# Performance work log

Measured on AMD Instinct MI355X. Metric: run time of the kernel, lower is better.

The kernel has to match this reference:

```python
import jax, jax.numpy as jnp
import numpy as np

N_NODES = 100000
N_EDGES = 1600000
IN_FEATS = 128
H_FEATS = 64
PROP_STEP = 2


def _gcn_propagate(x, src, dst, num_nodes, add_self_loops):
    """PyG gcn_norm + scatter-add propagation. edge_weight=None -> all ones.
    GCNConv uses add_self_loops=True; LGConv uses add_self_loops=False."""
    if add_self_loops:
        loop = jnp.arange(num_nodes, dtype=src.dtype)
        src = jnp.concatenate([src, loop])
        dst = jnp.concatenate([dst, loop])
    # degree over destination nodes (flow source_to_target)
    deg = jax.ops.segment_sum(jnp.ones(src.shape, dtype=x.dtype), dst,
                              num_segments=num_nodes)
    dinv = jnp.where(deg > 0, jax.lax.rsqrt(deg), jnp.zeros_like(deg))
    norm = dinv[src] * dinv[dst]                      # [E]
    msg = x[src] * norm[:, None]                      # [E, F] gather + scale
    return jax.ops.segment_sum(msg, dst, num_segments=num_nodes)  # [N, F]


def setup_inputs() -> dict:
    key = jax.random.key(0)
    k1, k2, k3 = jax.random.split(key, 3)
    edge_index = jax.random.randint(k1, (2, N_EDGES), 0, N_NODES, dtype=jnp.int32)
    in_feat = jax.random.normal(k2, (N_NODES, IN_FEATS), dtype=jnp.float32)
    # GCNConv linear weight (bias=False), stored as [in, out]
    W1 = jax.random.normal(k3, (IN_FEATS, H_FEATS), dtype=jnp.float32) * (1.0 / np.sqrt(IN_FEATS))
    alphas = jnp.ones((PROP_STEP,), dtype=jnp.float32)  # nn.Parameter(ones(prop_step))
    return {"edge_index": edge_index, "in_feat": in_feat, "W1": W1, "alphas": alphas}


def reference(edge_index, in_feat, W1, alphas):
    src, dst = edge_index[0], edge_index[1]
    num_nodes = in_feat.shape[0]
    alpha = jax.nn.softmax(alphas)
    # conv1 = GCNConv(bias=False): linear transform then normalized propagation with self loops
    h = _gcn_propagate(in_feat @ W1, src, dst, num_nodes, add_self_loops=True)
    res = h * alpha[0]
    # remaining steps: LGConv (no self loops), norm/relu disabled by default
    for i in range(1, PROP_STEP):
        h = _gcn_propagate(h, src, dst, num_nodes, add_self_loops=False)
        res = res + h * alpha[i]
    return res
```

## Files before the change

kernel.cpp:

```cpp
#include <hip/hip_runtime.h>

#define N_NODES 100000
#define N_EDGES 1600000
#define IN_F 128
#define H_F 64
#define ZROW N_NODES

#define BSH 10
#define BNODES 1024
#define NBKT 98
#define EPB 4096
#define BCAP 20000
#define SCAP 28192

typedef short short8 __attribute__((ext_vector_type(8)));
typedef float floatx4 __attribute__((ext_vector_type(4)));

union U16x8 { short8 v; unsigned short us[8]; unsigned int u[4]; };

static __device__ __forceinline__ unsigned short f2bf(float f) {
    unsigned int u = __float_as_uint(f);
    unsigned int r = (u + 0x7FFFu + ((u >> 16) & 1u)) >> 16;
    return (unsigned short)r;
}
static __device__ __forceinline__ float bflo(unsigned int u) {
    return __uint_as_float(u << 16);
}
static __device__ __forceinline__ float bfhi(unsigned int u) {
    return __uint_as_float(u & 0xFFFF0000u);
}
static __device__ __forceinline__ unsigned int pk2(float a, float b) {
    return (unsigned int)f2bf(a) | ((unsigned int)f2bf(b) << 16);
}

__global__ __launch_bounds__(256) void initwpack_kernel(const float* __restrict__ W,
                                                        unsigned int* __restrict__ wfrag,
                                                        int* __restrict__ ccur,
                                                        unsigned int* __restrict__ XsZ,
                                                        unsigned int* __restrict__ h1sZ) {
    int i = blockIdx.x * 256 + threadIdx.x;
    int reg = i & 3, lane = (i >> 2) & 63, fkc = i >> 8;
    int ct = fkc >> 2, kc = fkc & 3;
    int fcol = ct * 16 + (lane & 15);
    int k = kc * 32 + (lane >> 4) * 8 + reg * 2;
    wfrag[i] = pk2(W[k * 64 + fcol], W[(k + 1) * 64 + fcol]);

    if (blockIdx.x == 0) {
        int t = threadIdx.x;
        if (t < NBKT) ccur[t] = t * BCAP;
        if (t < 32) XsZ[t] = 0;
        else if (t < 64) h1sZ[t - 32] = 0;
    }
}

__global__ __launch_bounds__(256) void coarse_scatter_kernel(const int* __restrict__ src,
                                                             const int* __restrict__ dst,
                                                             int* __restrict__ ccur,
                                                             unsigned int* __restrict__ tmp, int E) {
    __shared__ unsigned int buf[EPB];
    __shared__ unsigned char bktA[EPB];
    __shared__ int cnt[NBKT], lofs[NBKT], gofs[NBKT];
    int base = blockIdx.x * EPB;
    int n = E - base; if (n > EPB) n = EPB;

    for (int i = threadIdx.x; i < NBKT; i += 256) cnt[i] = 0;
    __syncthreads();

    unsigned int v[16]; int bk[16], loc[16];
    #pragma unroll
    for (int j = 0; j < 16; ++j) {
        int o = threadIdx.x + j * 256;
        bk[j] = -1;
        if (o < n) {
            int s = src[base + o];
            int d = dst[base + o];
            bk[j]  = d >> BSH;
            v[j]   = ((unsigned int)(d & (BNODES - 1)) << 17) | (unsigned int)s;
            loc[j] = atomicAdd(&cnt[bk[j]], 1);
        }
    }
    __syncthreads();
    if (threadIdx.x == 0) {
        int run = 0;
        for (int b = 0; b < NBKT; ++b) { lofs[b] = run; run += cnt[b]; }
    }
    __syncthreads();
    if (threadIdx.x < NBKT && cnt[threadIdx.x] > 0)
        gofs[threadIdx.x] = atomicAdd(&ccur[threadIdx.x], cnt[threadIdx.x]);
    __syncthreads();
    #pragma unroll
    for (int j = 0; j < 16; ++j)
        if (bk[j] >= 0) {
            int p = lofs[bk[j]] + loc[j];
            buf[p]  = v[j];
            bktA[p] = (unsigned char)bk[j];
        }
    __syncthreads();
    for (int i = threadIdx.x; i < n; i += 256) {
        int b = bktA[i];
        tmp[gofs[b] + (i - lofs[b])] = buf[i];
    }
}

__global__ __launch_bounds__(512) void bucket_kernel(const unsigned int* __restrict__ tmp,
                                                     const int* __restrict__ ccur,
                                                     int* __restrict__ offsets,
                                                     unsigned char* __restrict__ npad8,
                                                     int* __restrict__ sorted_src,
                                                     float* __restrict__ dinv1,
                                                     float* __restrict__ dinv2, int N) {
    __shared__ int cnt[BNODES];
    __shared__ int sd[512];
    int b   = blockIdx.x;
    int tid = threadIdx.x;
    int tbeg = b * BCAP, tend = ccur[b];
    int sbase = b * SCAP;

    for (int i = tid; i < BNODES; i += 512) cnt[i] = 0;
    __syncthreads();
    for (int i = tbeg + tid; i < tend; i += 512)
        atomicAdd(&cnt[tmp[i] >> 17], 1);
    __syncthreads();

    int c0 = cnt[2 * tid], c1 = cnt[2 * tid + 1];
    int p0 = (c0 + 7) & ~7, p1 = (c1 + 7) & ~7;
    int s  = p0 + p1;
    sd[tid] = s;
    __syncthreads();
    for (int off = 1; off < 512; off <<= 1) {
        int t = (tid >= off) ? sd[tid - off] : 0;
        __syncthreads();
        sd[tid] += t;
        __syncthreads();
    }
    int ex = sd[tid] - s;
    int g0 = sbase + ex, g1 = sbase + ex + p0;

    int node0 = b * BNODES + 2 * tid;
    if (node0 < N) {
        offsets[node0] = g0;
        npad8[node0] = (unsigned char)(p0 >> 3);
        dinv1[node0] = rsqrtf((float)(c0 + 1));
        dinv2[node0] = c0 ? rsqrtf((float)c0) : 0.0f;
        for (int k = c0; k < p0; ++k) sorted_src[g0 + k] = ZROW;
    }
    if (node0 + 1 < N) {
        offsets[node0 + 1] = g1;
        npad8[node0 + 1] = (unsigned char)(p1 >> 3);
        dinv1[node0 + 1] = rsqrtf((float)(c1 + 1));
        dinv2[node0 + 1] = c1 ? rsqrtf((float)c1) : 0.0f;
        for (int k = c1; k < p1; ++k) sorted_src[g1 + k] = ZROW;
    }
    __syncthreads();
    cnt[2 * tid] = g0;
    cnt[2 * tid + 1] = g1;
    __syncthreads();

    for (int i = tbeg + tid; i < tend; i += 512) {
        unsigned int v = tmp[i];
        int p = atomicAdd(&cnt[v >> 17], 1);
        sorted_src[p] = (int)(v & 0x1FFFFu);
    }
}

__global__ __launch_bounds__(256) void gemm_kernel(const float* __restrict__ A,
                                                   const uint4* __restrict__ wfrag,
                                                   const float* __restrict__ dinv1,
                                                   unsigned short* __restrict__ Xs, int nTiles) {
    int wid = blockIdx.x * 4 + (threadIdx.x >> 6);
    int lane = threadIdx.x & 63;
    int lrow = lane & 15, lk = lane >> 4;

    short8 wf[16];
    #pragma unroll
    for (int i = 0; i < 16; ++i)
        wf[i] = *reinterpret_cast<const short8*>(&wfrag[i * 64 + lane]);

    #pragma unroll
    for (int tt = 0; tt < 4; ++tt) {
        int t = wid * 4 + tt;
        if (t >= nTiles) break;
        int node = t * 16 + lrow;
        const float4* ap = reinterpret_cast<const float4*>(A + (size_t)node * IN_F);

        short8 af[4];
        #pragma unroll
        for (int kc = 0; kc < 4; ++kc) {
            float4 x = ap[kc * 8 + lk * 2];
            float4 y = ap[kc * 8 + lk * 2 + 1];
            U16x8 u;
            u.us[0] = f2bf(x.x); u.us[1] = f2bf(x.y); u.us[2] = f2bf(x.z); u.us[3] = f2bf(x.w);
            u.us[4] = f2bf(y.x); u.us[5] = f2bf(y.y); u.us[6] = f2bf(y.z); u.us[7] = f2bf(y.w);
            af[kc] = u.v;
        }

        float dv = dinv1[node];
        #pragma unroll
        for (int ct = 0; ct < 4; ++ct) {
            floatx4 acc = {0.f, 0.f, 0.f, 0.f};
            acc = __builtin_amdgcn_mfma_f32_16x16x32_bf16(wf[ct * 4 + 0], af[0], acc, 0, 0, 0);
            acc = __builtin_amdgcn_mfma_f32_16x16x32_bf16(wf[ct * 4 + 1], af[1], acc, 0, 0, 0);
            acc = __builtin_amdgcn_mfma_f32_16x16x32_bf16(wf[ct * 4 + 2], af[2], acc, 0, 0, 0);
            acc = __builtin_amdgcn_mfma_f32_16x16x32_bf16(wf[ct * 4 + 3], af[3], acc, 0, 0, 0);
            uint2 o;
            o.x = pk2(acc[0] * dv, acc[1] * dv);
            o.y = pk2(acc[2] * dv, acc[3] * dv);
            *reinterpret_cast<uint2*>(Xs + (size_t)node * H_F + ct * 16 + lk * 4) = o;
        }
    }
}

__global__ __launch_bounds__(256) void prop1_kernel(const int* __restrict__ offsets,
                                                    const unsigned char* __restrict__ npad8,
                                                    const int* __restrict__ sorted_src,
                                                    const unsigned short* __restrict__ Xs,
                                                    const float* __restrict__ dinv1,
                                                    const float* __restrict__ dinv2,
                                                    unsigned short* __restrict__ h1,
                                                    unsigned short* __restrict__ h1s, int N) {
    int wid  = (blockIdx.x * blockDim.x + threadIdx.x) >> 6;
    int lane = threadIdx.x & 63;
    int g = lane >> 4, fl = lane & 15;
    int d = wid * 4 + g;
    bool active = d < N;
    int dd = active ? d : N - 1;

    int beg = offsets[dd];
    int nit = npad8[dd];
    const int* idp = sorted_src + beg;
    const char* XsB = (const char*)Xs;
    unsigned bo = (unsigned)(fl << 3);
    float c0 = 0.f, c1 = 0.f, c2 = 0.f, c3 = 0.f;

    for (int it = 0; it < nit; ++it, idp += 8) {
        int s[8]; uint2 v[8];
        #pragma unroll
        for (int j = 0; j < 8; ++j) s[j] = idp[j];
        #pragma unroll
        for (int j = 0; j < 8; ++j)
            v[j] = *reinterpret_cast<const uint2*>(XsB + (((unsigned)s[j] << 7) + bo));
        #pragma unroll
        for (int j = 0; j < 8; ++j) {
            c0 += bflo(v[j].x); c1 += bfhi(v[j].x); c2 += bflo(v[j].y); c3 += bfhi(v[j].y);
        }
    }

    float dv  = dinv1[dd];
    float dv2 = dinv2[dd];
    uint2 sv = *reinterpret_cast<const uint2*>(XsB + (((unsigned)dd << 7) + bo));
    float h0  = dv * (c0 + bflo(sv.x));
    float h1v = dv * (c1 + bfhi(sv.x));
    float h2  = dv * (c2 + bflo(sv.y));
    float h3  = dv * (c3 + bfhi(sv.y));
    if (active) {
        uint2 o1; o1.x = pk2(h0, h1v); o1.y = pk2(h2, h3);
        *reinterpret_cast<uint2*>(h1 + ((size_t)d << 6) + (fl << 2)) = o1;
        uint2 o2; o2.x = pk2(h0 * dv2, h1v * dv2); o2.y = pk2(h2 * dv2, h3 * dv2);
        *reinterpret_cast<uint2*>(h1s + ((size_t)d << 6) + (fl << 2)) = o2;
    }
}

__global__ __launch_bounds__(256) void prop2_kernel(const int* __restrict__ offsets,
                                                    const unsigned char* __restrict__ npad8,
                                                    const int* __restrict__ sorted_src,
                                                    const unsigned short* __restrict__ h1,
                                                    const unsigned short* __restrict__ h1s,
                                                    const float* __restrict__ dinv2,
                                                    const float* __restrict__ alphas,
                                                    float* __restrict__ out, int N) {
    int wid  = (blockIdx.x * blockDim.x + threadIdx.x) >> 6;
    int lane = threadIdx.x & 63;
    int g = lane >> 4, fl = lane & 15;
    int d = wid * 4 + g;
    bool active = d < N;
    int dd = active ? d : N - 1;

    float e0 = expf(alphas[0]), e1 = expf(alphas[1]);
    float aw0 = e0 / (e0 + e1), aw1 = e1 / (e0 + e1);

    int beg = offsets[dd];
    int nit = npad8[dd];
    const int* idp = sorted_src + beg;
    const char* HB = (const char*)h1s;
    unsigned bo = (unsigned)(fl << 3);
    float c0 = 0.f, c1 = 0.f, c2 = 0.f, c3 = 0.f;

    for (int it = 0; it < nit; ++it, idp += 8) {
        int s[8]; uint2 v[8];
        #pragma unroll
        for (int j = 0; j < 8; ++j) s[j] = idp[j];
        #pragma unroll
        for (int j = 0; j < 8; ++j)
            v[j] = *reinterpret_cast<const uint2*>(HB + (((unsigned)s[j] << 7) + bo));
        #pragma unroll
        for (int j = 0; j < 8; ++j) {
            c0 += bflo(v[j].x); c1 += bfhi(v[j].x); c2 += bflo(v[j].y); c3 += bfhi(v[j].y);
        }
    }

    if (active) {
        float sa1 = aw1 * dinv2[dd];
        uint2 sv = *reinterpret_cast<const uint2*>((const char*)h1 + (((unsigned)d << 7) + bo));
        float4 o;
        o.x = aw0 * bflo(sv.x) + sa1 * c0;
        o.y = aw0 * bfhi(sv.x) + sa1 * c1;
        o.z = aw0 * bflo(sv.y) + sa1 * c2;
        o.w = aw0 * bfhi(sv.y) + sa1 * c3;
        *reinterpret_cast<float4*>(out + ((size_t)d << 6) + (fl << 2)) = o;
    }
}

extern "C" void kernel_launch(void* const* d_in, const int* in_sizes, int n_in,
                              void* d_out, int out_size, void* d_ws, size_t ws_size,
                              hipStream_t stream) {
    const int*   edge_index = (const int*)d_in[0];
    const float* in_feat    = (const float*)d_in[1];
    const float* W1         = (const float*)d_in[2];
    const float* alphas     = (const float*)d_in[3];
    float*       out        = (float*)d_out;

    const int* src = edge_index;
    const int* dst = edge_index + N_EDGES;

    char* ws = (char*)d_ws;
    size_t tabBytes = (size_t)(N_NODES + 16) * H_F * 2;
    unsigned short* Xs  = (unsigned short*)(ws);
    unsigned int*   tmp = (unsigned int*)(ws);
    unsigned short* h1  = (unsigned short*)(ws + tabBytes);
    unsigned short* h1s = (unsigned short*)(ws + 2 * tabBytes);
    char* p = ws + 3 * tabBytes;
    int*   sorted = (int*)p;   p += (size_t)NBKT * SCAP * 4;
    int*   offs   = (int*)p;   p += (size_t)(N_NODES + 4) * 4;
    float* dinv1  = (float*)p; p += (size_t)N_NODES * 4;
    float* dinv2  = (float*)p; p += (size_t)N_NODES * 4;
    unsigned char* npad8 = (unsigned char*)p; p += (size_t)(N_NODES + 64);
    p = (char*)(((size_t)p + 63) & ~(size_t)63);
    int*   ccur   = (int*)p;   p += (size_t)NBKT * 4;
    unsigned int* wfrag = (unsigned int*)p; p += 8192 * 4;

    initwpack_kernel<<<32, 256, 0, stream>>>(W1, wfrag, ccur,
                                             (unsigned int*)(Xs + (size_t)N_NODES * H_F),
                                             (unsigned int*)(h1s + (size_t)N_NODES * H_F));
    coarse_scatter_kernel<<<(N_EDGES + EPB - 1) / EPB, 256, 0, stream>>>(src, dst, ccur, tmp, N_EDGES);
    bucket_kernel<<<NBKT, 512, 0, stream>>>(tmp, ccur, offs, npad8, sorted, dinv1, dinv2, N_NODES);

    int nTiles = N_NODES / 16;
    int gemm_waves = (nTiles + 3) / 4;
    gemm_kernel<<<(gemm_waves + 3) / 4, 256, 0, stream>>>(in_feat, (const uint4*)wfrag, dinv1, Xs, nTiles);

    int pwaves  = (N_NODES + 3) / 4;
    int pblocks = (pwaves + 3) / 4;
    prop1_kernel<<<pblocks, 256, 0, stream>>>(offs, npad8, sorted, Xs, dinv1, dinv2, h1, h1s, N_NODES);
    prop2_kernel<<<pblocks, 256, 0, stream>>>(offs, npad8, sorted, h1, h1s, dinv2, alphas, out, N_NODES);
}
```

Baseline: 129.4 us.

## Sort nodes by padded degree within buckets to balance propagation waves

The bucket kernel now builds a per-bucket histogram of padded neighbor counts and writes a permutation that groups nodes of similar degree together. Both propagation kernels process nodes in this permuted order, so the four 16-lane groups in a wave have similar loop trip counts and less divergence. The cost is an extra indirection load per node, plus scattered output writes and self-row reads, and a serial 64-entry prefix scan per block.

```diff
diff --git a/kernel.cpp b/kernel.cpp
--- a/kernel.cpp
+++ b/kernel.cpp
@@ -108,9 +108,11 @@
                                                      unsigned char* __restrict__ npad8,
                                                      int* __restrict__ sorted_src,
                                                      float* __restrict__ dinv1,
-                                                     float* __restrict__ dinv2, int N) {
+                                                     float* __restrict__ dinv2,
+                                                     int* __restrict__ perm, int N) {
     __shared__ int cnt[BNODES];
     __shared__ int sd[512];
+    __shared__ int dhist[64], dbase[64];
     int b   = blockIdx.x;
     int tid = threadIdx.x;
     int tbeg = b * BCAP, tend = ccur[b];
@@ -135,6 +137,8 @@
     }
     int ex = sd[tid] - s;
     int g0 = sbase + ex, g1 = sbase + ex + p0;
+
+    if (tid < 64) dhist[tid] = 0;
 
     int node0 = b * BNODES + 2 * tid;
     if (node0 < N) {
@@ -152,9 +156,21 @@
         for (int k = c1; k < p1; ++k) sorted_src[g1 + k] = ZROW;
     }
     __syncthreads();
+
+    int bin0 = p0 >> 3; if (bin0 > 63) bin0 = 63;
+    int bin1 = p1 >> 3; if (bin1 > 63) bin1 = 63;
+    if (node0 < N) atomicAdd(&dhist[bin0], 1);
+    if (node0 + 1 < N) atomicAdd(&dhist[bin1], 1);
     cnt[2 * tid] = g0;
     cnt[2 * tid + 1] = g1;
     __syncthreads();
+    if (tid == 0) {
+        int run = 0;
+        for (int q = 0; q < 64; ++q) { dbase[q] = run; run += dhist[q]; }
+    }
+    __syncthreads();
+    if (node0 < N) { int r = atomicAdd(&dbase[bin0], 1); perm[b * BNODES + r] = node0; }
+    if (node0 + 1 < N) { int r = atomicAdd(&dbase[bin1], 1); perm[b * BNODES + r] = node0 + 1; }
 
     for (int i = tbeg + tid; i < tend; i += 512) {
         unsigned int v = tmp[i];
@@ -210,7 +226,8 @@
     }
 }
 
-__global__ __launch_bounds__(256) void prop1_kernel(const int* __restrict__ offsets,
+__global__ __launch_bounds__(256) void prop1_kernel(const int* __restrict__ perm,
+                                                    const int* __restrict__ offsets,
                                                     const unsigned char* __restrict__ npad8,
                                                     const int* __restrict__ sorted_src,
                                                     const unsigned short* __restrict__ Xs,
@@ -221,12 +238,12 @@
     int wid  = (blockIdx.x * blockDim.x + threadIdx.x) >> 6;
     int lane = threadIdx.x & 63;
     int g = lane >> 4, fl = lane & 15;
-    int d = wid * 4 + g;
-    bool active = d < N;
-    int dd = active ? d : N - 1;
-
-    int beg = offsets[dd];
-    int nit = npad8[dd];
+    int slot = wid * 4 + g;
+    bool active = slot < N;
+    int d = perm[active ? slot : N - 1];
+
+    int beg = offsets[d];
+    int nit = npad8[d];
     const int* idp = sorted_src + beg;
     const char* XsB = (const char*)Xs;
     unsigned bo = (unsigned)(fl << 3);
@@ -245,9 +262,9 @@
         }
     }
 
-    float dv  = dinv1[dd];
-    float dv2 = dinv2[dd];
-    uint2 sv = *reinterpret_cast<const uint2*>(XsB + (((unsigned)dd << 7) + bo));
+    float dv  = dinv1[d];
+    float dv2 = dinv2[d];
+    uint2 sv = *reinterpret_cast<const uint2*>(XsB + (((unsigned)d << 7) + bo));
     float h0  = dv * (c0 + bflo(sv.x));
     float h1v = dv * (c1 + bfhi(sv.x));
     float h2  = dv * (c2 + bflo(sv.y));
@@ -260,7 +277,8 @@
     }
 }
 
-__global__ __launch_bounds__(256) void prop2_kernel(const int* __restrict__ offsets,
+__global__ __launch_bounds__(256) void prop2_kernel(const int* __restrict__ perm,
+                                                    const int* __restrict__ offsets,
                                                     const unsigned char* __restrict__ npad8,
                                                     const int* __restrict__ sorted_src,
                                                     const unsigned short* __restrict__ h1,
@@ -271,15 +289,15 @@
     int wid  = (blockIdx.x * blockDim.x + threadIdx.x) >> 6;
     int lane = threadIdx.x & 63;
     int g = lane >> 4, fl = lane & 15;
-    int d = wid * 4 + g;
-    bool active = d < N;
-    int dd = active ? d : N - 1;
+    int slot = wid * 4 + g;
+    bool active = slot < N;
+    int d = perm[active ? slot : N - 1];
 
     float e0 = expf(alphas[0]), e1 = expf(alphas[1]);
     float aw0 = e0 / (e0 + e1), aw1 = e1 / (e0 + e1);
 
-    int beg = offsets[dd];
-    int nit = npad8[dd];
+    int beg = offsets[d];
+    int nit = npad8[d];
     const int* idp = sorted_src + beg;
     const char* HB = (const char*)h1s;
     unsigned bo = (unsigned)(fl << 3);
@@ -299,7 +317,7 @@
     }
 
     if (active) {
-        float sa1 = aw1 * dinv2[dd];
+        float sa1 = aw1 * dinv2[d];
         uint2 sv = *reinterpret_cast<const uint2*>((const char*)h1 + (((unsigned)d << 7) + bo));
         float4 o;
         o.x = aw0 * bflo(sv.x) + sa1 * c0;
@@ -333,6 +351,7 @@
     int*   offs   = (int*)p;   p += (size_t)(N_NODES + 4) * 4;
     float* dinv1  = (float*)p; p += (size_t)N_NODES * 4;
     float* dinv2  = (float*)p; p += (size_t)N_NODES * 4;
+    int*   perm   = (int*)p;   p += (size_t)N_NODES * 4;
     unsigned char* npad8 = (unsigned char*)p; p += (size_t)(N_NODES + 64);
     p = (char*)(((size_t)p + 63) & ~(size_t)63);
     int*   ccur   = (int*)p;   p += (size_t)NBKT * 4;
@@ -342,7 +361,7 @@
                                              (unsigned int*)(Xs + (size_t)N_NODES * H_F),
                                              (unsigned int*)(h1s + (size_t)N_NODES * H_F));
     coarse_scatter_kernel<<<(N_EDGES + EPB - 1) / EPB, 256, 0, stream>>>(src, dst, ccur, tmp, N_EDGES);
-    bucket_kernel<<<NBKT, 512, 0, stream>>>(tmp, ccur, offs, npad8, sorted, dinv1, dinv2, N_NODES);
+    bucket_kernel<<<NBKT, 512, 0, stream>>>(tmp, ccur, offs, npad8, sorted, dinv1, dinv2, perm, N_NODES);
 
     int nTiles = N_NODES / 16;
     int gemm_waves = (nTiles + 3) / 4;
@@ -350,6 +369,6 @@
 
     int pwaves  = (N_NODES + 3) / 4;
     int pblocks = (pwaves + 3) / 4;
-    prop1_kernel<<<pblocks, 256, 0, stream>>>(offs, npad8, sorted, Xs, dinv1, dinv2, h1, h1s, N_NODES);
-    prop2_kernel<<<pblocks, 256, 0, stream>>>(offs, npad8, sorted, h1, h1s, dinv2, alphas, out, N_NODES);
-}
+    prop1_kernel<<<pblocks, 256, 0, stream>>>(perm, offs, npad8, sorted, Xs, dinv1, dinv2, h1, h1s, N_NODES);
+    prop2_kernel<<<pblocks, 256, 0, stream>>>(perm, offs, npad8, sorted, h1, h1s, dinv2, alphas, out, N_NODES);
+}
```

New measurement: 138.0 us, median of 2. +6.7%, slower.
